# Performance work log

Hardware: AMD Instinct MI355X
Metric: run time of the kernel (lower is better)

Reference implementation:

```python
import jax, jax.numpy as jnp
import numpy as np
from jax.ops import segment_sum, segment_max

N, E = 50000, 800000
IN_FEATS, H, D_HID, N_CLASSES = 256, 4, 32, 47
NEG_SLOPE = 0.2


def leaky_relu(x, slope=NEG_SLOPE):
    return jnp.where(x >= 0, x, slope * x)


def gat_conv(h, W, attn_l, attn_r, src, dst, n_nodes, heads, d_out):
    # h: [N, F_in]; W: [F_in, heads*d_out]; attn_l/attn_r: [heads, d_out]
    feat = (h @ W).reshape(n_nodes, heads, d_out)          # [N, H, D]
    el = jnp.sum(feat * attn_l, axis=-1)                   # [N, H]
    er = jnp.sum(feat * attn_r, axis=-1)                   # [N, H]
    e = leaky_relu(el[src] + er[dst])                      # [E, H]
    # segment softmax over incoming edges of each dst node
    e_max = segment_max(e, dst, num_segments=n_nodes)      # [N, H]
    e_exp = jnp.exp(e - e_max[dst])                        # [E, H]
    denom = segment_sum(e_exp, dst, num_segments=n_nodes)  # [N, H]
    alpha = e_exp / denom[dst]                             # [E, H]
    msg = feat[src] * alpha[..., None]                     # [E, H, D]
    return segment_sum(msg, dst, num_segments=n_nodes)     # [N, H, D]


def setup_inputs() -> dict:
    key = jax.random.key(0)
    ks = jax.random.split(key, 12)
    hd = H * D_HID
    def glorot(k, shape):
        fan = shape[0] + shape[-1] if len(shape) == 2 else int(np.prod(shape))
        return jax.random.normal(k, shape, dtype=jnp.float32) * np.sqrt(2.0 / fan)
    return {
        "x": jax.random.normal(ks[0], (N, IN_FEATS), dtype=jnp.float32),
        "src": jax.random.randint(ks[1], (E,), 0, N),
        "dst": jax.random.randint(ks[2], (E,), 0, N),
        "W1": glorot(ks[3], (IN_FEATS, hd)),
        "al1": glorot(ks[4], (H, D_HID)),
        "ar1": glorot(ks[5], (H, D_HID)),
        "W2": glorot(ks[6], (hd, hd)),
        "al2": glorot(ks[7], (H, D_HID)),
        "ar2": glorot(ks[8], (H, D_HID)),
        "W3": glorot(ks[9], (hd, H * N_CLASSES)),
        "al3": glorot(ks[10], (H, N_CLASSES)),
        "ar3": glorot(ks[11], (H, N_CLASSES)),
    }


def reference(x, src, dst, W1, al1, ar1, W2, al2, ar2, W3, al3, ar3):
    # layer 1: ELU activation, flatten heads
    h = gat_conv(x, W1, al1, ar1, src, dst, N, H, D_HID)
    h = jax.nn.elu(h).reshape(N, H * D_HID)
    # layer 2
    h = gat_conv(h, W2, al2, ar2, src, dst, N, H, D_HID)
    h = jax.nn.elu(h).reshape(N, H * D_HID)
    # layer 3: no activation, mean over heads, log softmax
    h = gat_conv(h, W3, al3, ar3, src, dst, N, H, N_CLASSES)
    h = h.mean(axis=1)                                      # [N, n_classes]
    return jax.nn.log_softmax(h, axis=-1)
```

## Files before the change

kernel.cpp:

```cpp
#include <hip/hip_runtime.h>
#include <hip/hip_bf16.h>
#include <math.h>
#include <string.h>

#define N_NODES 50000
#define N_EDGES 800000
#define NH 4
#define LSTR 68

typedef unsigned int u32;
typedef unsigned short u16;
typedef __attribute__((ext_vector_type(8))) short bf16x8;
typedef __attribute__((ext_vector_type(4))) float f32x4;
typedef __attribute__((ext_vector_type(2))) float f32x2;

__device__ __forceinline__ u32 pack_bf2(float a, float b) {
    __hip_bfloat162 h2 = __float22bfloat162_rn(make_float2(a, b));
    u32 r;
    memcpy(&r, &h2, 4);
    return r;
}
__device__ __forceinline__ f32x2 bf2_to_v2(u32 u) {
    f32x2 v;
    v.x = __uint_as_float(u << 16);
    v.y = __uint_as_float(u & 0xffff0000u);
    return v;
}
__device__ __forceinline__ short bf16r(float f) {
    __hip_bfloat16 h = __float2bfloat16(f);
    short s;
    memcpy(&s, &h, 2);
    return s;
}
__device__ __forceinline__ void pkfma_lo(f32x2& acc, f32x2 a, f32x2 b) {
    asm("v_pk_fma_f32 %0, %1, %2, %0 op_sel:[0,0,0] op_sel_hi:[0,1,1]"
        : "+v"(acc) : "v"(a), "v"(b));
}
__device__ __forceinline__ void pkfma_hi(f32x2& acc, f32x2 a, f32x2 b) {
    asm("v_pk_fma_f32 %0, %1, %2, %0 op_sel:[1,0,0] op_sel_hi:[1,1,1]"
        : "+v"(acc) : "v"(a), "v"(b));
}

__device__ __forceinline__ float wred_max(float v) {
#pragma unroll
    for (int o = 32; o > 0; o >>= 1) v = fmaxf(v, __shfl_xor(v, o));
    return v;
}
__device__ __forceinline__ float wred_sum(float v) {
#pragma unroll
    for (int o = 32; o > 0; o >>= 1) v += __shfl_xor(v, o);
    return v;
}


__global__ void k_hist(const int* __restrict__ dst, int* __restrict__ deg) {
    int i = blockIdx.x * 256 + threadIdx.x;
    if (i < N_EDGES) atomicAdd(&deg[dst[i]], 1);
}

__global__ __launch_bounds__(1024) void k_scan1(const int* __restrict__ deg,
                                                int* __restrict__ offs,
                                                int* __restrict__ bsum) {
    __shared__ int tmp[1024];
    int b = blockIdx.x, t = threadIdx.x;
    int i = b * 1024 + t;
    int v = (i < N_NODES) ? deg[i] : 0;
    tmp[t] = v;
    __syncthreads();
    for (int off = 1; off < 1024; off <<= 1) {
        int add = (t >= off) ? tmp[t - off] : 0;
        __syncthreads();
        tmp[t] += add;
        __syncthreads();
    }
    if (i < N_NODES) offs[i] = tmp[t] - v;
    if (t == 1023) bsum[b] = tmp[t];
}

__global__ void k_scan2(int* __restrict__ bsum, int nb) {
    int t = threadIdx.x & 63;
    int v = (t < nb) ? bsum[t] : 0;
    int orig = v;
#pragma unroll
    for (int o = 1; o < 64; o <<= 1) {
        int u = __shfl_up(v, o);
        if (t >= o) v += u;
    }
    if (t < nb) bsum[t] = v - orig;
}

__global__ __launch_bounds__(1024) void k_scan3(int* __restrict__ offs,
                                                const int* __restrict__ bsum,
                                                int* __restrict__ cursor) {
    int b = blockIdx.x, t = threadIdx.x;
    int i = b * 1024 + t;
    if (i < N_NODES) {
        int o = offs[i] + bsum[b];
        offs[i] = o;
        cursor[i] = o;
    }
    if (b == 0 && t == 0) offs[N_NODES] = N_EDGES;
}

__global__ void k_scatter(const int* __restrict__ src, const int* __restrict__ dst,
                          int* __restrict__ cursor, int* __restrict__ csrc) {
    int i = blockIdx.x * 256 + threadIdx.x;
    if (i < N_EDGES) {
        int p = atomicAdd(&cursor[dst[i]], 1);
        csrc[p] = src[i];
    }
}

__device__ __forceinline__ u16 pack_elem(const float* W, int i, int K, int NT, int NOUT) {
    int j = i & 7;
    int lane = (i >> 3) & 63;
    int rest = i >> 9;
    int nt = rest % NT;
    int kt = rest / NT;
    int k = kt * 32 + (lane >> 4) * 8 + j;
    int col = nt * 16 + (lane & 15);
    float v = (col < NOUT) ? W[(size_t)k * NOUT + col] : 0.f;
    return (u16)bf16r(v);
}
__device__ __forceinline__ u16 pack_elem3(const float* W, int i) {
    int j = i & 7;
    int lane = (i >> 3) & 63;
    int rest = i >> 9;
    int nt = rest % 12;
    int kt = rest / 12;
    int k = kt * 32 + (lane >> 4) * 8 + j;
    int col = nt * 16 + (lane & 15);
    int h = col / 48, d = col % 48;
    float v = (d < 47) ? W[(size_t)k * 188 + h * 47 + d] : 0.f;
    return (u16)bf16r(v);
}
__global__ void prep_all(const float* __restrict__ W1, const float* __restrict__ W2,
                         const float* __restrict__ W3, u16* __restrict__ wp1,
                         u16* __restrict__ wp2, u16* __restrict__ wp3) {
    int idx = blockIdx.x * 256 + threadIdx.x;
    if (idx < 32768) {
        wp1[idx] = pack_elem(W1, idx, 256, 8, 128);
    } else if (idx < 49152) {
        int i = idx - 32768;
        wp2[i] = pack_elem(W2, i, 128, 8, 128);
    } else if (idx < 73728) {
        int i = idx - 49152;
        wp3[i] = pack_elem3(W3, i);
    }
}

template <int K, int NOUT, int NP, bool AF32, bool DOTS, bool HEADPAD>
__global__ __launch_bounds__(256) void gemm_mfma(const void* __restrict__ Av,
                                                 const u16* __restrict__ Wp,
                                                 u16* __restrict__ feat,
                                                 const float* __restrict__ al,
                                                 const float* __restrict__ ar,
                                                 float* __restrict__ el,
                                                 float* __restrict__ er) {
    constexpr int NT = NP / 16;
    constexpr int KT = K / 32;
    int w = threadIdx.x >> 6, l = threadIdx.x & 63;
    int tile_m0 = blockIdx.x * 64 + w * 16;
    int c15 = l & 15;
    int rowA = tile_m0 + c15;
    if (rowA >= N_NODES) rowA = N_NODES - 1;
    int g = l >> 4;

    f32x4 acc[NT];
#pragma unroll
    for (int nt = 0; nt < NT; ++nt) acc[nt] = (f32x4){0.f, 0.f, 0.f, 0.f};

    for (int kt = 0; kt < KT; ++kt) {
        bf16x8 a;
        if constexpr (AF32) {
            const float* ap = (const float*)Av + (size_t)rowA * K + kt * 32 + g * 8;
            float4 f0 = *reinterpret_cast<const float4*>(ap);
            float4 f1 = *reinterpret_cast<const float4*>(ap + 4);
            a[0] = bf16r(f0.x); a[1] = bf16r(f0.y); a[2] = bf16r(f0.z); a[3] = bf16r(f0.w);
            a[4] = bf16r(f1.x); a[5] = bf16r(f1.y); a[6] = bf16r(f1.z); a[7] = bf16r(f1.w);
        } else {
            a = *reinterpret_cast<const bf16x8*>((const u16*)Av + (size_t)rowA * K + kt * 32 + g * 8);
        }
        const u16* wp = Wp + ((size_t)kt * NT) * 512 + (size_t)l * 8;
#pragma unroll
        for (int nt = 0; nt < NT; ++nt) {
            bf16x8 b = *reinterpret_cast<const bf16x8*>(wp + nt * 512);
            acc[nt] = __builtin_amdgcn_mfma_f32_16x16x32_bf16(a, b, acc[nt], 0, 0, 0);
        }
    }

    int rowD0 = tile_m0 + g * 4;
#pragma unroll
    for (int nt = 0; nt < NT; ++nt) {
        int col = nt * 16 + c15;
#pragma unroll
        for (int r = 0; r < 4; ++r) {
            int row = rowD0 + r;
            if (row < N_NODES)
                feat[(size_t)row * NP + col] = (u16)bf16r(acc[nt][r]);
        }
    }

    if constexpr (DOTS) {
        float alv[NT], arv[NT];
#pragma unroll
        for (int nt = 0; nt < NT; ++nt) {
            if constexpr (HEADPAD) {
                int h = nt / 3, m = nt % 3;
                if (m == 2) {
                    alv[nt] = (c15 < 15) ? al[h * 47 + 32 + c15] : 0.f;
                    arv[nt] = (c15 < 15) ? ar[h * 47 + 32 + c15] : 0.f;
                } else {
                    alv[nt] = al[h * 47 + m * 16 + c15];
                    arv[nt] = ar[h * 47 + m * 16 + c15];
                }
            } else {
                alv[nt] = al[nt * 16 + c15];
                arv[nt] = ar[nt * 16 + c15];
            }
        }
#pragma unroll
        for (int r = 0; r < 4; ++r) {
            float hlv[NH] = {0.f, 0.f, 0.f, 0.f};
            float hrv[NH] = {0.f, 0.f, 0.f, 0.f};
#pragma unroll
            for (int nt = 0; nt < NT; ++nt) {
                constexpr int NTH = NT / NH;
                int h = nt / NTH;
                hlv[h] = fmaf(acc[nt][r], alv[nt], hlv[h]);
                hrv[h] = fmaf(acc[nt][r], arv[nt], hrv[h]);
            }
#pragma unroll
            for (int o = 1; o < 16; o <<= 1) {
#pragma unroll
                for (int j = 0; j < NH; ++j) {
                    hlv[j] += __shfl_xor(hlv[j], o);
                    hrv[j] += __shfl_xor(hrv[j], o);
                }
            }
            int row = rowD0 + r;
            if (c15 == 0 && row < N_NODES) {
                *reinterpret_cast<float4*>(el + (size_t)row * NH) =
                    make_float4(hlv[0], hlv[1], hlv[2], hlv[3]);
                *reinterpret_cast<float4*>(er + (size_t)row * NH) =
                    make_float4(hrv[0], hrv[1], hrv[2], hrv[3]);
            }
        }
    }
}

__device__ __forceinline__ void alpha_chunk_T(const float* __restrict__ el,
                                              const int* __restrict__ csrc,
                                              float4 erv, int base, int i1,
                                              float4 mref, float4 vinv, bool online,
                                              float* __restrict__ lalT,
                                              int* __restrict__ lsrc, int lane) {
    int e = base + lane;
    bool act = e < i1;
    int srcn = act ? csrc[e] : 0;
    float4 elv = make_float4(0.f, 0.f, 0.f, 0.f);
    if (act) elv = *reinterpret_cast<const float4*>(el + (size_t)srcn * NH);
    float e0 = elv.x + erv.x; e0 = e0 >= 0.f ? e0 : 0.2f * e0;
    float e1 = elv.y + erv.y; e1 = e1 >= 0.f ? e1 : 0.2f * e1;
    float e2 = elv.z + erv.z; e2 = e2 >= 0.f ? e2 : 0.2f * e2;
    float e3 = elv.w + erv.w; e3 = e3 >= 0.f ? e3 : 0.2f * e3;
    float4 a4;
    if (online) {
        const float NEG = -__builtin_inff();
        float f0 = act ? e0 : NEG, f1 = act ? e1 : NEG, f2 = act ? e2 : NEG, f3 = act ? e3 : NEG;
        float m0 = wred_max(f0), m1 = wred_max(f1), m2 = wred_max(f2), m3 = wred_max(f3);
        float p0 = act ? __expf(e0 - m0) : 0.f;
        float p1 = act ? __expf(e1 - m1) : 0.f;
        float p2 = act ? __expf(e2 - m2) : 0.f;
        float p3 = act ? __expf(e3 - m3) : 0.f;
        float s0 = wred_sum(p0), s1 = wred_sum(p1), s2 = wred_sum(p2), s3 = wred_sum(p3);
        a4 = make_float4(act ? p0 / s0 : 0.f, act ? p1 / s1 : 0.f,
                         act ? p2 / s2 : 0.f, act ? p3 / s3 : 0.f);
    } else {
        a4 = make_float4(act ? __expf(e0 - mref.x) * vinv.x : 0.f,
                         act ? __expf(e1 - mref.y) * vinv.y : 0.f,
                         act ? __expf(e2 - mref.z) * vinv.z : 0.f,
                         act ? __expf(e3 - mref.w) * vinv.w : 0.f);
    }
    lalT[0 * LSTR + lane] = a4.x;
    lalT[1 * LSTR + lane] = a4.y;
    lalT[2 * LSTR + lane] = a4.z;
    lalT[3 * LSTR + lane] = a4.w;
    lsrc[lane] = srcn;
}

__device__ __forceinline__ void stats_pass(const float* __restrict__ el,
                                           const int* __restrict__ csrc,
                                           float4 erv, int i0, int i1, int lane,
                                           float4& mout, float4& vout) {
    const float NEG = -__builtin_inff();
    float m0 = NEG, m1 = NEG, m2 = NEG, m3 = NEG;
    float s0 = 0.f, s1 = 0.f, s2 = 0.f, s3 = 0.f;
    for (int base = i0; base < i1; base += 64) {
        int i = base + lane;
        bool act = i < i1;
        int srcn = act ? csrc[i] : 0;
        float4 elv = make_float4(0.f, 0.f, 0.f, 0.f);
        if (act) elv = *reinterpret_cast<const float4*>(el + (size_t)srcn * NH);
        float e0 = elv.x + erv.x; e0 = e0 >= 0.f ? e0 : 0.2f * e0;
        float e1 = elv.y + erv.y; e1 = e1 >= 0.f ? e1 : 0.2f * e1;
        float e2 = elv.z + erv.z; e2 = e2 >= 0.f ? e2 : 0.2f * e2;
        float e3 = elv.w + erv.w; e3 = e3 >= 0.f ? e3 : 0.2f * e3;
        if (!act) { e0 = NEG; e1 = NEG; e2 = NEG; e3 = NEG; }
        float c0 = wred_max(e0), c1 = wred_max(e1), c2 = wred_max(e2), c3 = wred_max(e3);
        float nm0 = fmaxf(m0, c0), nm1 = fmaxf(m1, c1), nm2 = fmaxf(m2, c2), nm3 = fmaxf(m3, c3);
        float p0 = act ? __expf(e0 - nm0) : 0.f;
        float p1 = act ? __expf(e1 - nm1) : 0.f;
        float p2 = act ? __expf(e2 - nm2) : 0.f;
        float p3 = act ? __expf(e3 - nm3) : 0.f;
        float S0 = wred_sum(p0), S1 = wred_sum(p1), S2 = wred_sum(p2), S3 = wred_sum(p3);
        s0 = s0 * __expf(m0 - nm0) + S0; m0 = nm0;
        s1 = s1 * __expf(m1 - nm1) + S1; m1 = nm1;
        s2 = s2 * __expf(m2 - nm2) + S2; m2 = nm2;
        s3 = s3 * __expf(m3 - nm3) + S3; m3 = nm3;
    }
    mout = make_float4(m0, m1, m2, m3);
    vout = make_float4(1.f / s0, 1.f / s1, 1.f / s2, 1.f / s3);
}

__global__ __launch_bounds__(256) void gat_agg128(const u16* __restrict__ feat,
                                                  const float* __restrict__ el,
                                                  const float* __restrict__ er,
                                                  const int* __restrict__ offs,
                                                  const int* __restrict__ csrc,
                                                  u16* __restrict__ out) {
    __shared__ float lalT[4][4][LSTR];
    __shared__ int lsrc[4][64];
    int wave = threadIdx.x >> 6;
    int lane = threadIdx.x & 63;
    int n = blockIdx.x * 4 + wave;
    int h = lane >> 4;
    u32 lo4 = (u32)lane * 4u;
    int i0 = offs[n], i1 = offs[n + 1];
    int d = i1 - i0;
    f32x2 acc = (f32x2){0.f, 0.f};
    if (d > 0) {
        float4 erv = *reinterpret_cast<const float4*>(er + (size_t)n * NH);
        float4 mref = make_float4(0.f, 0.f, 0.f, 0.f), vinv = mref;
        bool onechunk = d <= 64;
        if (!onechunk) stats_pass(el, csrc, erv, i0, i1, lane, mref, vinv);
        const char* fbase = (const char*)feat;
        for (int base = i0; base < i1; base += 64) {
            alpha_chunk_T(el, csrc, erv, base, i1, mref, vinv, onechunk,
                          &lalT[wave][0][0], &lsrc[wave][0], lane);
            int cnt = i1 - base; if (cnt > 64) cnt = 64;
            int cpad = (cnt + 3) & ~3;
            for (int j = 0; j < cpad; j += 4) {
                int4 sv = *reinterpret_cast<const int4*>(&lsrc[wave][j]);
                float4 aq = *reinterpret_cast<const float4*>(&lalT[wave][h][j]);
                f32x2 aqLo = (f32x2){aq.x, aq.y};
                f32x2 aqHi = (f32x2){aq.z, aq.w};
                u32 o0 = ((u32)sv.x << 8) + lo4;
                u32 o1 = ((u32)sv.y << 8) + lo4;
                u32 o2 = ((u32)sv.z << 8) + lo4;
                u32 o3 = ((u32)sv.w << 8) + lo4;
                u32 q0 = *reinterpret_cast<const u32*>(fbase + o0);
                u32 q1 = *reinterpret_cast<const u32*>(fbase + o1);
                u32 q2 = *reinterpret_cast<const u32*>(fbase + o2);
                u32 q3 = *reinterpret_cast<const u32*>(fbase + o3);
                pkfma_lo(acc, aqLo, bf2_to_v2(q0));
                pkfma_hi(acc, aqLo, bf2_to_v2(q1));
                pkfma_lo(acc, aqHi, bf2_to_v2(q2));
                pkfma_hi(acc, aqHi, bf2_to_v2(q3));
            }
        }
    }
    float ox = acc.x > 0.f ? acc.x : expm1f(acc.x);
    float oy = acc.y > 0.f ? acc.y : expm1f(acc.y);
    *reinterpret_cast<u32*>(out + (size_t)n * 128 + 2 * lane) = pack_bf2(ox, oy);
}

__global__ __launch_bounds__(256) void gat_agg_final(const u16* __restrict__ feat,
                                                     const float* __restrict__ el,
                                                     const float* __restrict__ er,
                                                     const int* __restrict__ offs,
                                                     const int* __restrict__ csrc,
                                                     float* __restrict__ out) {
    __shared__ float lalT[4][4][LSTR];
    __shared__ int lsrc[4][64];
    __shared__ float lds[4][192];
    int wave = threadIdx.x >> 6;
    int lane = threadIdx.x & 63;
    int n = blockIdx.x * 4 + wave;
    int e0 = 2 * lane;
    bool up = lane < 32;
    int hLo = e0 / 48;
    int hHi = up ? (128 + e0) / 48 : 3;
    u32 lo4 = (u32)lane * 4u;
    int i0 = offs[n], i1 = offs[n + 1];
    int d = i1 - i0;
    f32x2 accLo = (f32x2){0.f, 0.f};
    f32x2 accHi = (f32x2){0.f, 0.f};
    if (d > 0) {
        float4 erv = *reinterpret_cast<const float4*>(er + (size_t)n * NH);
        float4 mref = make_float4(0.f, 0.f, 0.f, 0.f), vinv = mref;
        bool onechunk = d <= 64;
        if (!onechunk) stats_pass(el, csrc, erv, i0, i1, lane, mref, vinv);
        const char* fbase = (const char*)feat;
        for (int base = i0; base < i1; base += 64) {
            alpha_chunk_T(el, csrc, erv, base, i1, mref, vinv, onechunk,
                          &lalT[wave][0][0], &lsrc[wave][0], lane);
            int cnt = i1 - base; if (cnt > 64) cnt = 64;
            int cpad = (cnt + 3) & ~3;
            for (int j = 0; j < cpad; j += 4) {
                int4 sv = *reinterpret_cast<const int4*>(&lsrc[wave][j]);
                float4 wlo = *reinterpret_cast<const float4*>(&lalT[wave][hLo][j]);
                float4 whi = *reinterpret_cast<const float4*>(&lalT[wave][hHi][j]);
                f32x2 wloA = (f32x2){wlo.x, wlo.y};
                f32x2 wloB = (f32x2){wlo.z, wlo.w};
                f32x2 whiA = (f32x2){whi.x, whi.y};
                f32x2 whiB = (f32x2){whi.z, whi.w};
                u32 oA = (u32)sv.x * 384u + lo4;
                u32 oB = (u32)sv.y * 384u + lo4;
                u32 oC = (u32)sv.z * 384u + lo4;
                u32 oD = (u32)sv.w * 384u + lo4;
                u32 a0 = *reinterpret_cast<const u32*>(fbase + oA);
                u32 b0 = *reinterpret_cast<const u32*>(fbase + oB);
                u32 c0 = *reinterpret_cast<const u32*>(fbase + oC);
                u32 d0 = *reinterpret_cast<const u32*>(fbase + oD);
                u32 a1 = up ? *reinterpret_cast<const u32*>(fbase + oA + 256) : 0u;
                u32 b1 = up ? *reinterpret_cast<const u32*>(fbase + oB + 256) : 0u;
                u32 c1 = up ? *reinterpret_cast<const u32*>(fbase + oC + 256) : 0u;
                u32 d1 = up ? *reinterpret_cast<const u32*>(fbase + oD + 256) : 0u;
                pkfma_lo(accLo, wloA, bf2_to_v2(a0));
                pkfma_hi(accLo, wloA, bf2_to_v2(b0));
                pkfma_lo(accLo, wloB, bf2_to_v2(c0));
                pkfma_hi(accLo, wloB, bf2_to_v2(d0));
                pkfma_lo(accHi, whiA, bf2_to_v2(a1));
                pkfma_hi(accHi, whiA, bf2_to_v2(b1));
                pkfma_lo(accHi, whiB, bf2_to_v2(c1));
                pkfma_hi(accHi, whiB, bf2_to_v2(d1));
            }
        }
    }
    lds[wave][e0] = accLo.x;
    lds[wave][e0 + 1] = accLo.y;
    if (up) {
        lds[wave][128 + e0] = accHi.x;
        lds[wave][129 + e0] = accHi.y;
    }
    __syncthreads();
    float u = (lane < 47)
                  ? 0.25f * (lds[wave][lane] + lds[wave][48 + lane] +
                             lds[wave][96 + lane] + lds[wave][144 + lane])
                  : -__builtin_inff();
    float mx = u;
#pragma unroll
    for (int o = 32; o > 0; o >>= 1) mx = fmaxf(mx, __shfl_xor(mx, o));
    float ex = (lane < 47) ? __expf(u - mx) : 0.f;
    float sm = ex;
#pragma unroll
    for (int o = 32; o > 0; o >>= 1) sm += __shfl_xor(sm, o);
    if (lane < 47) out[(size_t)n * 47 + lane] = u - mx - logf(sm);
}


extern "C" void kernel_launch(void* const* d_in, const int* in_sizes, int n_in,
                              void* d_out, int out_size, void* d_ws, size_t ws_size,
                              hipStream_t stream) {
    const float* x = (const float*)d_in[0];
    const int* src = (const int*)d_in[1];
    const int* dst = (const int*)d_in[2];
    const float* W1 = (const float*)d_in[3];
    const float* al1 = (const float*)d_in[4];
    const float* ar1 = (const float*)d_in[5];
    const float* W2 = (const float*)d_in[6];
    const float* al2 = (const float*)d_in[7];
    const float* ar2 = (const float*)d_in[8];
    const float* W3 = (const float*)d_in[9];
    const float* al3 = (const float*)d_in[10];
    const float* ar3 = (const float*)d_in[11];
    float* out = (float*)d_out;

    char* p = (char*)d_ws;
    auto alloc = [&](size_t bytes) {
        char* r = p;
        p += (bytes + 255) & ~(size_t)255;
        return r;
    };
    u16* bufA = (u16*)alloc((size_t)N_NODES * 128 * 2);
    u16* bufC = (u16*)alloc((size_t)N_NODES * 128 * 2);
    u16* featb = (u16*)alloc((size_t)N_NODES * 192 * 2);
    float* el = (float*)alloc((size_t)N_NODES * NH * 4);
    float* er = (float*)alloc((size_t)N_NODES * NH * 4);
    u16* wp1 = (u16*)alloc((size_t)32768 * 2);
    u16* wp2 = (u16*)alloc((size_t)16384 * 2);
    u16* wp3 = (u16*)alloc((size_t)24576 * 2);
    int* deg = (int*)alloc((size_t)N_NODES * 4);
    int* offs = (int*)alloc((size_t)(N_NODES + 1) * 4);
    int* cursor = (int*)alloc((size_t)N_NODES * 4);
    int* bsum = (int*)alloc(64 * 4);
    int* csrc = (int*)alloc((size_t)N_EDGES * 4);

    prep_all<<<288, 256, 0, stream>>>(W1, W2, W3, wp1, wp2, wp3);

    hipMemsetAsync(deg, 0, (size_t)N_NODES * 4, stream);
    k_hist<<<(N_EDGES + 255) / 256, 256, 0, stream>>>(dst, deg);
    k_scan1<<<49, 1024, 0, stream>>>(deg, offs, bsum);
    k_scan2<<<1, 64, 0, stream>>>(bsum, 49);
    k_scan3<<<49, 1024, 0, stream>>>(offs, bsum, cursor);
    k_scatter<<<(N_EDGES + 255) / 256, 256, 0, stream>>>(src, dst, cursor, csrc);

    int gemm_grid = (N_NODES + 63) / 64;
    gemm_mfma<256, 128, 128, true, true, false><<<gemm_grid, 256, 0, stream>>>(x, wp1, featb, al1, ar1, el, er);
    gat_agg128<<<N_NODES / 4, 256, 0, stream>>>(featb, el, er, offs, csrc, bufA);
    gemm_mfma<128, 128, 128, false, true, false><<<gemm_grid, 256, 0, stream>>>(bufA, wp2, featb, al2, ar2, el, er);
    gat_agg128<<<N_NODES / 4, 256, 0, stream>>>(featb, el, er, offs, csrc, bufC);
    gemm_mfma<128, 192, 192, false, true, true><<<gemm_grid, 256, 0, stream>>>(bufC, wp3, featb, al3, ar3, el, er);
    gat_agg_final<<<N_NODES / 4, 256, 0, stream>>>(featb, el, er, offs, csrc, out);
}
```

Measured before the change: 295.3 us.

## Use 16-byte feature gathers with edge-parallel subgroups and shuffle reduction

The aggregation kernels now split each wave into subgroups that each handle a different edge. Every lane loads 16 bytes (8 bf16 values) per edge instead of 4 bytes, and the partial sums are combined across subgroups with xor shuffles. Byte offsets are precomputed into shared memory so the inner loop does no multiplication. The aim is fewer, wider gather instructions and better memory-level parallelism, at the cost of extra shuffle reductions, more accumulator registers, and idle lanes in the final layer (24 of 32 active).

```diff
diff --git a/kernel.cpp b/kernel.cpp
--- a/kernel.cpp
+++ b/kernel.cpp
@@ -251,10 +251,10 @@
 
 __device__ __forceinline__ void alpha_chunk_T(const float* __restrict__ el,
                                               const int* __restrict__ csrc,
-                                              float4 erv, int base, int i1,
+                                              float4 erv, int base, int i1, u32 rowb,
                                               float4 mref, float4 vinv, bool online,
                                               float* __restrict__ lalT,
-                                              int* __restrict__ lsrc, int lane) {
+                                              u32* __restrict__ loff, int lane) {
     int e = base + lane;
     bool act = e < i1;
     int srcn = act ? csrc[e] : 0;
@@ -286,7 +286,7 @@
     lalT[1 * LSTR + lane] = a4.y;
     lalT[2 * LSTR + lane] = a4.z;
     lalT[3 * LSTR + lane] = a4.w;
-    lsrc[lane] = srcn;
+    loff[lane] = (u32)srcn * rowb;
 }
 
 __device__ __forceinline__ void stats_pass(const float* __restrict__ el,
@@ -330,15 +330,16 @@
                                                   const int* __restrict__ csrc,
                                                   u16* __restrict__ out) {
     __shared__ float lalT[4][4][LSTR];
-    __shared__ int lsrc[4][64];
+    __shared__ u32 loff[4][64];
     int wave = threadIdx.x >> 6;
     int lane = threadIdx.x & 63;
     int n = blockIdx.x * 4 + wave;
-    int h = lane >> 4;
-    u32 lo4 = (u32)lane * 4u;
+    int sub = lane >> 4, sl = lane & 15;
+    int h = sl >> 2;
+    u32 soff = (u32)sl * 16u;
     int i0 = offs[n], i1 = offs[n + 1];
     int d = i1 - i0;
-    f32x2 acc = (f32x2){0.f, 0.f};
+    f32x2 acc0 = (f32x2){0.f, 0.f}, acc1 = acc0, acc2 = acc0, acc3 = acc0;
     if (d > 0) {
         float4 erv = *reinterpret_cast<const float4*>(er + (size_t)n * NH);
         float4 mref = make_float4(0.f, 0.f, 0.f, 0.f), vinv = mref;
@@ -346,33 +347,41 @@
         if (!onechunk) stats_pass(el, csrc, erv, i0, i1, lane, mref, vinv);
         const char* fbase = (const char*)feat;
         for (int base = i0; base < i1; base += 64) {
-            alpha_chunk_T(el, csrc, erv, base, i1, mref, vinv, onechunk,
-                          &lalT[wave][0][0], &lsrc[wave][0], lane);
+            alpha_chunk_T(el, csrc, erv, base, i1, 256u, mref, vinv, onechunk,
+                          &lalT[wave][0][0], &loff[wave][0], lane);
             int cnt = i1 - base; if (cnt > 64) cnt = 64;
-            int cpad = (cnt + 3) & ~3;
-            for (int j = 0; j < cpad; j += 4) {
-                int4 sv = *reinterpret_cast<const int4*>(&lsrc[wave][j]);
-                float4 aq = *reinterpret_cast<const float4*>(&lalT[wave][h][j]);
-                f32x2 aqLo = (f32x2){aq.x, aq.y};
-                f32x2 aqHi = (f32x2){aq.z, aq.w};
-                u32 o0 = ((u32)sv.x << 8) + lo4;
-                u32 o1 = ((u32)sv.y << 8) + lo4;
-                u32 o2 = ((u32)sv.z << 8) + lo4;
-                u32 o3 = ((u32)sv.w << 8) + lo4;
-                u32 q0 = *reinterpret_cast<const u32*>(fbase + o0);
-                u32 q1 = *reinterpret_cast<const u32*>(fbase + o1);
-                u32 q2 = *reinterpret_cast<const u32*>(fbase + o2);
-                u32 q3 = *reinterpret_cast<const u32*>(fbase + o3);
-                pkfma_lo(acc, aqLo, bf2_to_v2(q0));
-                pkfma_hi(acc, aqLo, bf2_to_v2(q1));
-                pkfma_lo(acc, aqHi, bf2_to_v2(q2));
-                pkfma_hi(acc, aqHi, bf2_to_v2(q3));
+            int cpad = (cnt + 7) & ~7;
+            for (int j = 0; j < cpad; j += 8) {
+                u32 o0 = loff[wave][j + sub] + soff;
+                u32 o1 = loff[wave][j + 4 + sub] + soff;
+                uint4 q0 = *reinterpret_cast<const uint4*>(fbase + o0);
+                uint4 q1 = *reinterpret_cast<const uint4*>(fbase + o1);
+                f32x2 ap = (f32x2){lalT[wave][h][j + sub], lalT[wave][h][j + 4 + sub]};
+                pkfma_lo(acc0, ap, bf2_to_v2(q0.x));
+                pkfma_lo(acc1, ap, bf2_to_v2(q0.y));
+                pkfma_lo(acc2, ap, bf2_to_v2(q0.z));
+                pkfma_lo(acc3, ap, bf2_to_v2(q0.w));
+                pkfma_hi(acc0, ap, bf2_to_v2(q1.x));
+                pkfma_hi(acc1, ap, bf2_to_v2(q1.y));
+                pkfma_hi(acc2, ap, bf2_to_v2(q1.z));
+                pkfma_hi(acc3, ap, bf2_to_v2(q1.w));
             }
         }
     }
-    float ox = acc.x > 0.f ? acc.x : expm1f(acc.x);
-    float oy = acc.y > 0.f ? acc.y : expm1f(acc.y);
-    *reinterpret_cast<u32*>(out + (size_t)n * 128 + 2 * lane) = pack_bf2(ox, oy);
+    float v[8] = {acc0.x, acc0.y, acc1.x, acc1.y, acc2.x, acc2.y, acc3.x, acc3.y};
+#pragma unroll
+    for (int k = 0; k < 8; ++k) {
+        v[k] += __shfl_xor(v[k], 16);
+        v[k] += __shfl_xor(v[k], 32);
+    }
+    if (sub == 0) {
+        float o[8];
+#pragma unroll
+        for (int k = 0; k < 8; ++k) o[k] = v[k] > 0.f ? v[k] : expm1f(v[k]);
+        uint4 wv = make_uint4(pack_bf2(o[0], o[1]), pack_bf2(o[2], o[3]),
+                              pack_bf2(o[4], o[5]), pack_bf2(o[6], o[7]));
+        *reinterpret_cast<uint4*>(out + (size_t)n * 128 + sl * 8) = wv;
+    }
 }
 
 __global__ __launch_bounds__(256) void gat_agg_final(const u16* __restrict__ feat,
@@ -382,20 +391,18 @@
                                                      const int* __restrict__ csrc,
                                                      float* __restrict__ out) {
     __shared__ float lalT[4][4][LSTR];
-    __shared__ int lsrc[4][64];
+    __shared__ u32 loff[4][64];
     __shared__ float lds[4][192];
     int wave = threadIdx.x >> 6;
     int lane = threadIdx.x & 63;
     int n = blockIdx.x * 4 + wave;
-    int e0 = 2 * lane;
-    bool up = lane < 32;
-    int hLo = e0 / 48;
-    int hHi = up ? (128 + e0) / 48 : 3;
-    u32 lo4 = (u32)lane * 4u;
+    int sub = lane >> 5, sl = lane & 31;
+    bool act = sl < 24;
+    int h = act ? (sl / 6) : 0;
+    u32 soff = (u32)sl * 16u;
     int i0 = offs[n], i1 = offs[n + 1];
     int d = i1 - i0;
-    f32x2 accLo = (f32x2){0.f, 0.f};
-    f32x2 accHi = (f32x2){0.f, 0.f};
+    f32x2 acc0 = (f32x2){0.f, 0.f}, acc1 = acc0, acc2 = acc0, acc3 = acc0;
     if (d > 0) {
         float4 erv = *reinterpret_cast<const float4*>(er + (size_t)n * NH);
         float4 mref = make_float4(0.f, 0.f, 0.f, 0.f), vinv = mref;
@@ -403,46 +410,37 @@
         if (!onechunk) stats_pass(el, csrc, erv, i0, i1, lane, mref, vinv);
         const char* fbase = (const char*)feat;
         for (int base = i0; base < i1; base += 64) {
-            alpha_chunk_T(el, csrc, erv, base, i1, mref, vinv, onechunk,
-                          &lalT[wave][0][0], &lsrc[wave][0], lane);
+            alpha_chunk_T(el, csrc, erv, base, i1, 384u, mref, vinv, onechunk,
+                          &lalT[wave][0][0], &loff[wave][0], lane);
             int cnt = i1 - base; if (cnt > 64) cnt = 64;
             int cpad = (cnt + 3) & ~3;
-            for (int j = 0; j < cpad; j += 4) {
-                int4 sv = *reinterpret_cast<const int4*>(&lsrc[wave][j]);
-                float4 wlo = *reinterpret_cast<const float4*>(&lalT[wave][hLo][j]);
-                float4 whi = *reinterpret_cast<const float4*>(&lalT[wave][hHi][j]);
-                f32x2 wloA = (f32x2){wlo.x, wlo.y};
-                f32x2 wloB = (f32x2){wlo.z, wlo.w};
-                f32x2 whiA = (f32x2){whi.x, whi.y};
-                f32x2 whiB = (f32x2){whi.z, whi.w};
-                u32 oA = (u32)sv.x * 384u + lo4;
-                u32 oB = (u32)sv.y * 384u + lo4;
-                u32 oC = (u32)sv.z * 384u + lo4;
-                u32 oD = (u32)sv.w * 384u + lo4;
-                u32 a0 = *reinterpret_cast<const u32*>(fbase + oA);
-                u32 b0 = *reinterpret_cast<const u32*>(fbase + oB);
-                u32 c0 = *reinterpret_cast<const u32*>(fbase + oC);
-                u32 d0 = *reinterpret_cast<const u32*>(fbase + oD);
-                u32 a1 = up ? *reinterpret_cast<const u32*>(fbase + oA + 256) : 0u;
-                u32 b1 = up ? *reinterpret_cast<const u32*>(fbase + oB + 256) : 0u;
-                u32 c1 = up ? *reinterpret_cast<const u32*>(fbase + oC + 256) : 0u;
-                u32 d1 = up ? *reinterpret_cast<const u32*>(fbase + oD + 256) : 0u;
-                pkfma_lo(accLo, wloA, bf2_to_v2(a0));
-                pkfma_hi(accLo, wloA, bf2_to_v2(b0));
-                pkfma_lo(accLo, wloB, bf2_to_v2(c0));
-                pkfma_hi(accLo, wloB, bf2_to_v2(d0));
-                pkfma_lo(accHi, whiA, bf2_to_v2(a1));
-                pkfma_hi(accHi, whiA, bf2_to_v2(b1));
-                pkfma_lo(accHi, whiB, bf2_to_v2(c1));
-                pkfma_hi(accHi, whiB, bf2_to_v2(d1));
+            if (act) {
+                for (int j = 0; j < cpad; j += 4) {
+                    u32 o0 = loff[wave][j + sub] + soff;
+                    u32 o1 = loff[wave][j + 2 + sub] + soff;
+                    uint4 q0 = *reinterpret_cast<const uint4*>(fbase + o0);
+                    uint4 q1 = *reinterpret_cast<const uint4*>(fbase + o1);
+                    f32x2 ap = (f32x2){lalT[wave][h][j + sub], lalT[wave][h][j + 2 + sub]};
+                    pkfma_lo(acc0, ap, bf2_to_v2(q0.x));
+                    pkfma_lo(acc1, ap, bf2_to_v2(q0.y));
+                    pkfma_lo(acc2, ap, bf2_to_v2(q0.z));
+                    pkfma_lo(acc3, ap, bf2_to_v2(q0.w));
+                    pkfma_hi(acc0, ap, bf2_to_v2(q1.x));
+                    pkfma_hi(acc1, ap, bf2_to_v2(q1.y));
+                    pkfma_hi(acc2, ap, bf2_to_v2(q1.z));
+                    pkfma_hi(acc3, ap, bf2_to_v2(q1.w));
+                }
             }
         }
     }
-    lds[wave][e0] = accLo.x;
-    lds[wave][e0 + 1] = accLo.y;
-    if (up) {
-        lds[wave][128 + e0] = accHi.x;
-        lds[wave][129 + e0] = accHi.y;
+    float v[8] = {acc0.x, acc0.y, acc1.x, acc1.y, acc2.x, acc2.y, acc3.x, acc3.y};
+#pragma unroll
+    for (int k = 0; k < 8; ++k) v[k] += __shfl_xor(v[k], 32);
+    if (sub == 0 && act) {
+        float4 lo = make_float4(v[0], v[1], v[2], v[3]);
+        float4 hi = make_float4(v[4], v[5], v[6], v[7]);
+        *reinterpret_cast<float4*>(&lds[wave][sl * 8]) = lo;
+        *reinterpret_cast<float4*>(&lds[wave][sl * 8 + 4]) = hi;
     }
     __syncthreads();
     float u = (lane < 47)
```

Result: no change. 298.3 us (+1.0%).
